# Optimization experiments

Measured on AMD Instinct MI355X. Metric: run time of the kernel, lower is better.

Reference implementation:

```python
import jax, jax.numpy as jnp
import numpy as np

N, E, G = 100000, 1600000, 64   # nodes, edges, graphs
IN, H, OUT = 32, 128, 3


def setup_inputs() -> dict:
    key = jax.random.key(0)
    ks = jax.random.split(key, 24)
    def w(k, i, o):
        return (jax.random.normal(k, (i, o), jnp.float32) / np.sqrt(i)).astype(jnp.float32)
    inp = {
        "x": jax.random.normal(ks[0], (N, IN), jnp.float32),
        "edge_index": jax.random.randint(ks[1], (2, E), 0, N, dtype=jnp.int32).astype(jnp.int64),
        "batch": jnp.sort(jax.random.randint(ks[2], (N,), 0, G, dtype=jnp.int32)).astype(jnp.int64),
        # SAGEConv layer 0 (in->hidden): lin_l (neighbors, with bias), lin_r (root, no bias)
        "Wl0": w(ks[3], IN, H), "bl0": jnp.zeros((H,), jnp.float32), "Wr0": w(ks[4], IN, H),
        # SAGEConv layers 1,2 (hidden->hidden)
        "Wl1": w(ks[5], H, H), "bl1": jnp.zeros((H,), jnp.float32), "Wr1": w(ks[6], H, H),
        "Wl2": w(ks[7], H, H), "bl2": jnp.zeros((H,), jnp.float32), "Wr2": w(ks[8], H, H),
        # output head
        "Wfc": w(ks[9], H, OUT), "bfc": jnp.zeros((OUT,), jnp.float32),
        # aux MLP on (dim1, dim3)
        "Wa1": w(ks[10], 2, H), "ba1": jnp.zeros((H,), jnp.float32),
        "Wa2": w(ks[11], H, H), "ba2": jnp.zeros((H,), jnp.float32),
        "Wao": w(ks[12], H, 1), "bao": jnp.zeros((1,), jnp.float32),
    }
    return inp


def _sage_conv(x, src, dst, Wl, bl, Wr):
    # PyG SAGEConv (mean aggr): out = lin_l(mean_{j in N(i)} x_j) + lin_r(x_i)
    msg = x[src]                                   # [E, d] gather
    agg = jax.ops.segment_sum(msg, dst, num_segments=N)
    cnt = jax.ops.segment_sum(jnp.ones((src.shape[0],), x.dtype), dst, num_segments=N)
    mean = agg / jnp.maximum(cnt, 1.0)[:, None]
    return mean @ Wl + bl + x @ Wr


def reference(x, edge_index, batch,
              Wl0, bl0, Wr0, Wl1, bl1, Wr1, Wl2, bl2, Wr2,
              Wfc, bfc, Wa1, ba1, Wa2, ba2, Wao, bao):
    src, dst = edge_index[0], edge_index[1]
    h = jax.nn.relu(_sage_conv(x, src, dst, Wl0, bl0, Wr0))   # dropout is identity in eval
    h = jax.nn.relu(_sage_conv(h, src, dst, Wl1, bl1, Wr1))
    h = jax.nn.relu(_sage_conv(h, src, dst, Wl2, bl2, Wr2))
    main = h @ Wfc + bfc                                      # [N, 3]
    dim1, dim3 = main[:, 0], main[:, 2]
    aux_in = jnp.stack([dim1, dim3], axis=-1)                 # [N, 2]
    a = jax.nn.relu(aux_in @ Wa1 + ba1)
    a = jax.nn.relu(a @ Wa2 + ba2)
    aux_out = (a @ Wao + bao)[:, 0]                           # [N]
    final = jnp.stack([dim1, aux_out, dim3], axis=-1)         # [N, 3]
    # global mean pool over graph ids
    s = jax.ops.segment_sum(final, batch, num_segments=G)
    c = jax.ops.segment_sum(jnp.ones((final.shape[0],), final.dtype), batch, num_segments=G)
    return s / jnp.maximum(c, 1.0)[:, None]                   # [G, 3]
```

## Files before the change

kernel.cpp:

```cpp
#include <hip/hip_runtime.h>

#define NR 128
#define PART_CH 4096
typedef unsigned short ushortT;
typedef __attribute__((ext_vector_type(8))) short short8;
typedef __attribute__((ext_vector_type(4))) float float4v;
typedef __attribute__((ext_vector_type(2))) float float2v;

__device__ __forceinline__ unsigned short f32_to_bf16_rne(float f) {
    unsigned u = __float_as_uint(f);
    unsigned r = (u + 0x7fffu + ((u >> 16) & 1u)) >> 16;
    return (unsigned short)r;
}

__device__ __forceinline__ unsigned char f32_to_fp8(float f) {
    return (unsigned char)(__builtin_amdgcn_cvt_pk_fp8_f32(f, f, 0, false) & 0xff);
}

__device__ __forceinline__ void accum8(float* acc, uint4 v) {
    unsigned u[4] = {v.x, v.y, v.z, v.w};
#pragma unroll
    for (int q = 0; q < 4; q++) {
        acc[2 * q]     += __uint_as_float(u[q] << 16);
        acc[2 * q + 1] += __uint_as_float(u[q] & 0xffff0000u);
    }
}

__device__ __forceinline__ void accum32_fp8(float* ag, uint4 A, uint4 B) {
    unsigned w[8] = {A.x, A.y, A.z, A.w, B.x, B.y, B.z, B.w};
#pragma unroll
    for (int m = 0; m < 8; m++) {
        float2v lo = __builtin_amdgcn_cvt_pk_f32_fp8(w[m], false);
        float2v hi = __builtin_amdgcn_cvt_pk_f32_fp8(w[m], true);
        ag[4 * m + 0] += lo.x;
        ag[4 * m + 1] += lo.y;
        ag[4 * m + 2] += hi.x;
        ag[4 * m + 3] += hi.y;
    }
}


__launch_bounds__(256)
__global__ void bucket_count(const int* __restrict__ dst, int* __restrict__ bcnt, int E, int NB) {
    __shared__ int h[1024];
    int t = threadIdx.x;
    for (int j = t; j < NB; j += 256) h[j] = 0;
    __syncthreads();
    int e0 = blockIdx.x * PART_CH;
    int e1 = min(e0 + PART_CH, E);
    for (int base = e0; base < e1; base += 2048) {
        int idx = base + t;
        int d[8];
        int cnt = 0;
#pragma unroll
        for (int u = 0; u < 8; u++) {
            int e = idx + u * 256;
            if (e < e1) d[cnt++] = dst[e];
        }
        for (int u = 0; u < cnt; u++) atomicAdd(&h[d[u] >> 7], 1);
    }
    __syncthreads();
    for (int j = t; j < NB; j += 256) {
        int v = h[j];
        if (v) atomicAdd(&bcnt[j], v);
    }
}

__launch_bounds__(256)
__global__ void bucket_scan(const int* __restrict__ bcnt, int* __restrict__ bstart,
                            int* __restrict__ gcur, int NB, int E) {
    __shared__ int sh[256];
    int t = threadIdx.x;
    int v[4];
    int tot = 0;
#pragma unroll
    for (int j = 0; j < 4; j++) {
        int idx = t * 4 + j;
        v[j] = (idx < NB) ? bcnt[idx] : 0;
        tot += v[j];
    }
    sh[t] = tot;
    __syncthreads();
    for (int off = 1; off < 256; off <<= 1) {
        int add = (t >= off) ? sh[t - off] : 0;
        __syncthreads();
        sh[t] += add;
        __syncthreads();
    }
    int run = sh[t] - tot;
#pragma unroll
    for (int j = 0; j < 4; j++) {
        int idx = t * 4 + j;
        if (idx < NB) { bstart[idx] = run; gcur[idx] = run; }
        run += v[j];
    }
    if (t == 0) bstart[NB] = E;
}

__launch_bounds__(256)
__global__ void partition_edges(const int* __restrict__ src, const int* __restrict__ dst,
                                int* __restrict__ gcur, unsigned* __restrict__ packed,
                                int E, int NB) {
    __shared__ int hist[1024];
    __shared__ int base[1024];
    int t = threadIdx.x;
    int e0 = blockIdx.x * PART_CH;
    int e1 = min(e0 + PART_CH, E);
    for (int j = t; j < NB; j += 256) hist[j] = 0;
    __syncthreads();
    for (int bb = e0; bb < e1; bb += 2048) {
        int idx = bb + t;
        int d[8];
        int cnt = 0;
#pragma unroll
        for (int u = 0; u < 8; u++) {
            int e = idx + u * 256;
            if (e < e1) d[cnt++] = dst[e];
        }
        for (int u = 0; u < cnt; u++) atomicAdd(&hist[d[u] >> 7], 1);
    }
    __syncthreads();
    for (int j = t; j < NB; j += 256) {
        int h = hist[j];
        base[j] = h ? atomicAdd(&gcur[j], h) : 0;
    }
    __syncthreads();
    for (int j = t; j < NB; j += 256) hist[j] = base[j];
    __syncthreads();
    for (int bb = e0; bb < e1; bb += 2048) {
        int idx = bb + t;
        int d[8], s[8];
        int cnt = 0;
#pragma unroll
        for (int u = 0; u < 8; u++) {
            int e = idx + u * 256;
            if (e < e1) { d[cnt] = dst[e]; s[cnt] = src[e]; cnt++; }
        }
        for (int u = 0; u < cnt; u++) {
            int dd = d[u];
            int pos = atomicAdd(&hist[dd >> 7], 1);
            packed[pos] = (unsigned)s[u] | ((unsigned)(dd & (NR - 1)) << 17);
        }
    }
}

__launch_bounds__(256)
__global__ void bucket_sort(const unsigned* __restrict__ packed, const int* __restrict__ bstart,
                            int* __restrict__ row_start, int* __restrict__ srcs, int N) {
    __shared__ int cnt[1024];
    __shared__ int cur[1024];
    __shared__ int psum[256];
    int b = blockIdx.x, t = threadIdx.x;
    int nb0 = b * NR;
    int nnode = min(NR, N - nb0);
    int lo = bstart[b], hi = bstart[b + 1];
#pragma unroll
    for (int j = 0; j < 4; j++) cnt[t + j * 256] = 0;
    __syncthreads();
    for (int bb = lo; bb < hi; bb += 2048) {
        int idx = bb + t;
        unsigned pk[8];
        int c = 0;
#pragma unroll
        for (int u = 0; u < 8; u++) {
            int e = idx + u * 256;
            if (e < hi) pk[c++] = packed[e];
        }
        for (int u = 0; u < c; u++) {
            unsigned s = pk[u] & 0x1FFFFu;
            int key = (int)((pk[u] >> 17) << 3) | (int)(s >> 14);
            atomicAdd(&cnt[key], 1);
        }
    }
    __syncthreads();
    int base4 = t * 4;
    int v0 = cnt[base4], v1 = cnt[base4 + 1], v2 = cnt[base4 + 2], v3 = cnt[base4 + 3];
    int s4 = v0 + v1 + v2 + v3;
    psum[t] = s4;
    __syncthreads();
    for (int off = 1; off < 256; off <<= 1) {
        int add = (t >= off) ? psum[t - off] : 0;
        __syncthreads();
        psum[t] += add;
        __syncthreads();
    }
    int run = psum[t] - s4;
    cnt[base4]     = run;
    cnt[base4 + 1] = run + v0;
    cnt[base4 + 2] = run + v0 + v1;
    cnt[base4 + 3] = run + v0 + v1 + v2;
    cur[base4]     = lo + run;
    cur[base4 + 1] = lo + run + v0;
    cur[base4 + 2] = lo + run + v0 + v1;
    cur[base4 + 3] = lo + run + v0 + v1 + v2;
    __syncthreads();
    if (t < nnode) row_start[nb0 + t] = lo + cnt[t << 3];
    if (t == 0 && nb0 + nnode == N) row_start[N] = hi;
    __syncthreads();
    for (int bb = lo; bb < hi; bb += 2048) {
        int idx = bb + t;
        unsigned pk[8];
        int c = 0;
#pragma unroll
        for (int u = 0; u < 8; u++) {
            int e = idx + u * 256;
            if (e < hi) pk[c++] = packed[e];
        }
        for (int u = 0; u < c; u++) {
            unsigned s = pk[u] & 0x1FFFFu;
            int key = (int)((pk[u] >> 17) << 3) | (int)(s >> 14);
            int pos = atomicAdd(&cur[key], 1);
            srcs[pos] = (int)s;
        }
    }
}


__global__ void prep_fused(const float* __restrict__ x, ushortT* __restrict__ xbf, int n4,
                           const float* __restrict__ Wl0, const float* __restrict__ Wr0,
                           const float* __restrict__ Wl1, const float* __restrict__ Wr1,
                           const float* __restrict__ Wl2, const float* __restrict__ Wr2,
                           const float* __restrict__ Wa2,
                           ushortT* __restrict__ Wt0, ushortT* __restrict__ Wt1,
                           ushortT* __restrict__ Wt2, ushortT* __restrict__ Wa2t) {
    int tid0 = blockIdx.x * 256 + threadIdx.x;
    if (tid0 < n4) {
        float4 v = ((const float4*)x)[tid0];
        ushort4 o;
        o.x = f32_to_bf16_rne(v.x);
        o.y = f32_to_bf16_rne(v.y);
        o.z = f32_to_bf16_rne(v.z);
        o.w = f32_to_bf16_rne(v.w);
        ((ushort4*)xbf)[tid0] = o;
        return;
    }
    int tid = tid0 - n4;
    if (tid < 8192) {
        int col = tid >> 6, k = tid & 63;
        float v = (k < 32) ? Wl0[k * 128 + col] : Wr0[(k - 32) * 128 + col];
        Wt0[col * 64 + ((k + 8 * col) & 63)] = f32_to_bf16_rne(v);
    } else if (tid < 8192 + 32768) {
        int j = tid - 8192;
        int col = j >> 8, k = j & 255;
        float v = (k < 128) ? Wl1[k * 128 + col] : Wr1[(k - 128) * 128 + col];
        Wt1[(k >> 6) * 8192 + col * 64 + (((k & 63) + 8 * col) & 63)] = f32_to_bf16_rne(v);
    } else if (tid < 8192 + 65536) {
        int j = tid - 8192 - 32768;
        int col = j >> 8, k = j & 255;
        float v = (k < 128) ? Wl2[k * 128 + col] : Wr2[(k - 128) * 128 + col];
        Wt2[(k >> 6) * 8192 + col * 64 + (((k & 63) + 8 * col) & 63)] = f32_to_bf16_rne(v);
    } else if (tid < 8192 + 65536 + 16384) {
        int j = tid - 8192 - 65536;
        int col = j >> 7, k = j & 127;
        Wa2t[(k >> 6) * 8192 + col * 64 + (((k & 63) + 8 * col) & 63)] = f32_to_bf16_rne(Wa2[k * 128 + col]);
    }
}


__device__ __forceinline__ void gather_fp8(const uint4* __restrict__ hp,
                                           const int* __restrict__ srcs,
                                           int lo, int deg, int q, float* ag) {
    if (deg <= 0) return;
    int last = lo + deg - 1;
    int nb = (deg + 3) >> 2;
    int sA[4], sB[4];
    uint4 A[8], B[8];
#pragma unroll
    for (int u = 0; u < 4; u++) sA[u] = srcs[min(lo + u, last)];
#pragma unroll
    for (int u = 0; u < 4; u++) {
        size_t bs = (size_t)sA[u] * 8 + q * 2;
        A[2 * u] = hp[bs];
        A[2 * u + 1] = hp[bs + 1];
    }
#pragma unroll
    for (int u = 0; u < 4; u++) sB[u] = srcs[min(lo + 4 + u, last)];
    for (int b = 0; b < nb; b += 2) {
#pragma unroll
        for (int u = 0; u < 4; u++) {
            size_t bs = (size_t)sB[u] * 8 + q * 2;
            B[2 * u] = hp[bs];
            B[2 * u + 1] = hp[bs + 1];
        }
#pragma unroll
        for (int u = 0; u < 4; u++) sA[u] = srcs[min(lo + (b + 2) * 4 + u, last)];
        {
            int rem = deg - b * 4;
#pragma unroll
            for (int u = 0; u < 4; u++)
                if (u < rem) accum32_fp8(ag, A[2 * u], A[2 * u + 1]);
        }
#pragma unroll
        for (int u = 0; u < 4; u++) {
            size_t bs = (size_t)sA[u] * 8 + q * 2;
            A[2 * u] = hp[bs];
            A[2 * u + 1] = hp[bs + 1];
        }
#pragma unroll
        for (int u = 0; u < 4; u++) sB[u] = srcs[min(lo + (b + 3) * 4 + u, last)];
        {
            int rem = deg - (b + 1) * 4;
#pragma unroll
            for (int u = 0; u < 4; u++)
                if (u < rem) accum32_fp8(ag, B[2 * u], B[2 * u + 1]);
        }
    }
}

__device__ __forceinline__ void gather_bf16(const uint4* __restrict__ xp,
                                            const int* __restrict__ srcs,
                                            int lo, int deg, int q, float* ag) {
    if (deg <= 0) return;
    int last = lo + deg - 1;
    int nb = (deg + 7) >> 3;
    int sA[8], sB[8];
    uint4 A[8], B[8];
#pragma unroll
    for (int u = 0; u < 8; u++) sA[u] = srcs[min(lo + u, last)];
#pragma unroll
    for (int u = 0; u < 8; u++) A[u] = xp[(size_t)sA[u] * 4 + q];
#pragma unroll
    for (int u = 0; u < 8; u++) sB[u] = srcs[min(lo + 8 + u, last)];
    for (int b = 0; b < nb; b += 2) {
#pragma unroll
        for (int u = 0; u < 8; u++) B[u] = xp[(size_t)sB[u] * 4 + q];
#pragma unroll
        for (int u = 0; u < 8; u++) sA[u] = srcs[min(lo + (b + 2) * 8 + u, last)];
        {
            int rem = deg - b * 8;
#pragma unroll
            for (int u = 0; u < 8; u++)
                if (u < rem) accum8(ag, A[u]);
        }
#pragma unroll
        for (int u = 0; u < 8; u++) A[u] = xp[(size_t)sA[u] * 4 + q];
#pragma unroll
        for (int u = 0; u < 8; u++) sB[u] = srcs[min(lo + (b + 3) * 8 + u, last)];
        {
            int rem = deg - (b + 1) * 8;
#pragma unroll
            for (int u = 0; u < 8; u++)
                if (u < rem) accum8(ag, B[u]);
        }
    }
}


__device__ __forceinline__ void stage_copy(ushortT* sW, const ushortT* Wq, int t) {
    const uint4* Wg = (const uint4*)Wq;
    uint4* Ws = (uint4*)sW;
#pragma unroll
    for (int j = 0; j < 4; j++) Ws[t + j * 256] = Wg[t + j * 256];
}

template <int KH, bool IN_FP8>
__device__ __forceinline__ void gemm_agg_body(
        const void* __restrict__ gat, const ushortT* __restrict__ Ah,
        const int* __restrict__ srcs, const int* __restrict__ rs,
        const ushortT* __restrict__ Wt, const float* __restrict__ bias,
        ushortT* __restrict__ outbf, unsigned char* __restrict__ outf8, int n) {
    constexpr int NKS = KH / 32;
    __shared__ __attribute__((aligned(16))) ushortT sW[128 * 64];
    int t = threadIdx.x;
    stage_copy(sW, Wt, t);
    int wv = t >> 6, lane = t & 63;
    int q = lane >> 4, cid = lane & 15;
    int row = blockIdx.x * 64 + wv * 16 + cid;
    int rc = min(row, n - 1);

    float ag[NKS * 8];
#pragma unroll
    for (int j = 0; j < NKS * 8; j++) ag[j] = 0.f;
    int lo = rs[rc], deg = rs[rc + 1] - lo;
    if constexpr (IN_FP8) gather_fp8((const uint4*)gat, srcs, lo, deg, q, ag);
    else                  gather_bf16((const uint4*)gat, srcs, lo, deg, q, ag);
    float inv = 1.0f / (float)max(deg, 1);
    short8 am[NKS];
#pragma unroll
    for (int ks = 0; ks < NKS; ks++)
#pragma unroll
        for (int j = 0; j < 8; j++) am[ks][j] = (short)f32_to_bf16_rne(ag[ks * 8 + j] * inv);
    short8 ah[NKS];
#pragma unroll
    for (int ks = 0; ks < NKS; ks++)
        ah[ks] = *(const short8*)(Ah + (size_t)rc * KH + ks * 32 + q * 8);
    __syncthreads();

    float4v acc[8];
#pragma unroll
    for (int j = 0; j < 8; j++) acc[j] = (float4v){0.f, 0.f, 0.f, 0.f};
    int pbase = q * 8 + 8 * cid;
    if constexpr (KH == 32) {
        {
            int p = pbase & 63;
#pragma unroll
            for (int j = 0; j < 8; ++j) {
                short8 b = *(const short8*)(sW + (j * 16 + cid) * 64 + p);
                acc[j] = __builtin_amdgcn_mfma_f32_16x16x32_bf16(am[0], b, acc[j], 0, 0, 0);
            }
        }
        {
            int p = (32 + pbase) & 63;
#pragma unroll
            for (int j = 0; j < 8; ++j) {
                short8 b = *(const short8*)(sW + (j * 16 + cid) * 64 + p);
                acc[j] = __builtin_amdgcn_mfma_f32_16x16x32_bf16(ah[0], b, acc[j], 0, 0, 0);
            }
        }
    } else {
#pragma unroll
        for (int st = 0; st < 4; st++) {
            if (st > 0) {
                __syncthreads();
                stage_copy(sW, Wt + st * 8192, t);
                __syncthreads();
            }
#pragma unroll
            for (int ksl = 0; ksl < 2; ksl++) {
                short8 a = (st < 2) ? am[st * 2 + ksl] : ah[(st - 2) * 2 + ksl];
                int p = (ksl * 32 + pbase) & 63;
#pragma unroll
                for (int j = 0; j < 8; ++j) {
                    short8 b = *(const short8*)(sW + (j * 16 + cid) * 64 + p);
                    acc[j] = __builtin_amdgcn_mfma_f32_16x16x32_bf16(a, b, acc[j], 0, 0, 0);
                }
            }
        }
    }
    float bo[8];
#pragma unroll
    for (int j = 0; j < 8; ++j) bo[j] = bias[j * 16 + cid];
    int orow = blockIdx.x * 64 + wv * 16 + q * 4;
#pragma unroll
    for (int rr = 0; rr < 4; ++rr) {
        int r = orow + rr;
        if (r < n) {
#pragma unroll
            for (int j = 0; j < 8; ++j) {
                int col = j * 16 + cid;
                float v = fmaxf(acc[j][rr] + bo[j], 0.f);
                outbf[(size_t)r * 128 + col] = f32_to_bf16_rne(v);
                int pc = ((col >> 3) & 3) * 32 + ((col >> 5) << 3) + (col & 7);
                outf8[(size_t)r * 128 + pc] = f32_to_fp8(v);
            }
        }
    }
}

__launch_bounds__(256, 2)
__global__ void gemm_agg32(const void* __restrict__ gat, const ushortT* __restrict__ Ah,
                           const int* __restrict__ srcs, const int* __restrict__ rs,
                           const ushortT* __restrict__ Wt, const float* __restrict__ bias,
                           ushortT* __restrict__ outbf, unsigned char* __restrict__ outf8, int n) {
    gemm_agg_body<32, false>(gat, Ah, srcs, rs, Wt, bias, outbf, outf8, n);
}

__launch_bounds__(256, 2)
__global__ void gemm_agg128(const void* __restrict__ gat, const ushortT* __restrict__ Ah,
                            const int* __restrict__ srcs, const int* __restrict__ rs,
                            const ushortT* __restrict__ Wt, const float* __restrict__ bias,
                            ushortT* __restrict__ outbf, unsigned char* __restrict__ outf8, int n) {
    gemm_agg_body<128, true>(gat, Ah, srcs, rs, Wt, bias, outbf, outf8, n);
}


__launch_bounds__(256, 2)
__global__ void gemm_agg_fin(const void* __restrict__ gat, const ushortT* __restrict__ Ah,
                             const int* __restrict__ srcs, const int* __restrict__ rs,
                             const ushortT* __restrict__ Wt, const float* __restrict__ bias,
                             const float* __restrict__ Wfc, const float* __restrict__ bfc,
                             const ushortT* __restrict__ Wa2t, const float* __restrict__ Wa1,
                             const float* __restrict__ ba1, const float* __restrict__ ba2,
                             const float* __restrict__ Wao, const float* __restrict__ bao,
                             float* __restrict__ fin, int n) {
    __shared__ __attribute__((aligned(16))) ushortT sW[128 * 64];
    __shared__ float sD1[64], sD3[64];
    __shared__ float sWa1a[128], sWa1b[128], sBa1[128];
    int t = threadIdx.x;
    stage_copy(sW, Wt, t);
    if (t < 128) { sWa1a[t] = Wa1[t]; sWa1b[t] = Wa1[128 + t]; sBa1[t] = ba1[t]; }
    int wv = t >> 6, lane = t & 63;
    int q = lane >> 4, cid = lane & 15;
    int row = blockIdx.x * 64 + wv * 16 + cid;
    int rc = min(row, n - 1);

    float ag[32];
#pragma unroll
    for (int j = 0; j < 32; j++) ag[j] = 0.f;
    int lo = rs[rc], deg = rs[rc + 1] - lo;
    gather_fp8((const uint4*)gat, srcs, lo, deg, q, ag);
    float inv = 1.0f / (float)max(deg, 1);
    short8 am[4];
#pragma unroll
    for (int ks = 0; ks < 4; ks++)
#pragma unroll
        for (int j = 0; j < 8; j++) am[ks][j] = (short)f32_to_bf16_rne(ag[ks * 8 + j] * inv);
    short8 ah[4];
#pragma unroll
    for (int ks = 0; ks < 4; ks++)
        ah[ks] = *(const short8*)(Ah + (size_t)rc * 128 + ks * 32 + q * 8);
    __syncthreads();

    float4v acc[8];
#pragma unroll
    for (int j = 0; j < 8; j++) acc[j] = (float4v){0.f, 0.f, 0.f, 0.f};
    int pbase = q * 8 + 8 * cid;
#pragma unroll
    for (int st = 0; st < 4; st++) {
        if (st > 0) {
            __syncthreads();
            stage_copy(sW, Wt + st * 8192, t);
            __syncthreads();
        }
#pragma unroll
        for (int ksl = 0; ksl < 2; ksl++) {
            short8 a = (st < 2) ? am[st * 2 + ksl] : ah[(st - 2) * 2 + ksl];
            int p = (ksl * 32 + pbase) & 63;
#pragma unroll
            for (int j = 0; j < 8; ++j) {
                short8 b = *(const short8*)(sW + (j * 16 + cid) * 64 + p);
                acc[j] = __builtin_amdgcn_mfma_f32_16x16x32_bf16(a, b, acc[j], 0, 0, 0);
            }
        }
    }

    float bo[8], w1[8], w3[8];
#pragma unroll
    for (int j = 0; j < 8; ++j) {
        int col = j * 16 + cid;
        bo[j] = bias[col];
        w1[j] = Wfc[col * 3 + 0];
        w3[j] = Wfc[col * 3 + 2];
    }
    float bfc0 = bfc[0], bfc2 = bfc[2];
#pragma unroll
    for (int rr = 0; rr < 4; ++rr) {
        float p1 = 0.f, p3 = 0.f;
#pragma unroll
        for (int j = 0; j < 8; ++j) {
            float v = fmaxf(acc[j][rr] + bo[j], 0.f);
            p1 += v * w1[j];
            p3 += v * w3[j];
        }
        p1 += __shfl_xor(p1, 1, 64); p3 += __shfl_xor(p3, 1, 64);
        p1 += __shfl_xor(p1, 2, 64); p3 += __shfl_xor(p3, 2, 64);
        p1 += __shfl_xor(p1, 4, 64); p3 += __shfl_xor(p3, 4, 64);
        p1 += __shfl_xor(p1, 8, 64); p3 += __shfl_xor(p3, 8, 64);
        if (cid == 0) {
            int rowl = wv * 16 + q * 4 + rr;
            float d1 = p1 + bfc0, d3 = p3 + bfc2;
            sD1[rowl] = d1;
            sD3[rowl] = d3;
            int r = blockIdx.x * 64 + rowl;
            if (r < n) {
                fin[(size_t)r * 3 + 0] = d1;
                fin[(size_t)r * 3 + 2] = d3;
            }
        }
    }
    __syncthreads();

    int rl = wv * 16 + cid;
    float d1a = sD1[rl], d3a = sD3[rl];
    float4v hacc[8];
#pragma unroll
    for (int j = 0; j < 8; j++) hacc[j] = (float4v){0.f, 0.f, 0.f, 0.f};
#pragma unroll
    for (int hs = 0; hs < 2; hs++) {
        if (hs > 0) __syncthreads();
        stage_copy(sW, Wa2t + hs * 8192, t);
        __syncthreads();
#pragma unroll
        for (int ksl = 0; ksl < 2; ++ksl) {
            int k0 = hs * 64 + ksl * 32 + q * 8;
            short8 a0;
#pragma unroll
            for (int j = 0; j < 8; ++j) {
                int k = k0 + j;
                float v0 = fmaxf(fmaf(d1a, sWa1a[k], fmaf(d3a, sWa1b[k], sBa1[k])), 0.f);
                a0[j] = (short)f32_to_bf16_rne(v0);
            }
            int p = (ksl * 32 + pbase) & 63;
#pragma unroll
            for (int j = 0; j < 8; ++j) {
                short8 b = *(const short8*)(sW + (j * 16 + cid) * 64 + p);
                hacc[j] = __builtin_amdgcn_mfma_f32_16x16x32_bf16(a0, b, hacc[j], 0, 0, 0);
            }
        }
    }
    float b2[8], wo[8];
#pragma unroll
    for (int j = 0; j < 8; ++j) {
        int col = j * 16 + cid;
        b2[j] = ba2[col];
        wo[j] = Wao[col];
    }
    float bao0 = bao[0];
#pragma unroll
    for (int rr = 0; rr < 4; ++rr) {
        float s = 0.f;
#pragma unroll
        for (int j = 0; j < 8; ++j) s += fmaxf(hacc[j][rr] + b2[j], 0.f) * wo[j];
        s += __shfl_xor(s, 1, 64);
        s += __shfl_xor(s, 2, 64);
        s += __shfl_xor(s, 4, 64);
        s += __shfl_xor(s, 8, 64);
        int r = blockIdx.x * 64 + wv * 16 + q * 4 + rr;
        if (cid == 0 && r < n) fin[(size_t)r * 3 + 1] = s + bao0;
    }
}


__global__ void pool_kernel(const float* __restrict__ fin, const int* __restrict__ batch,
                            float* __restrict__ out, int n) {
    int g = blockIdx.x, t = threadIdx.x;
    int lo = 0, hi = n;
    while (lo < hi) { int mid = (lo + hi) >> 1; if (batch[mid] < g) lo = mid + 1; else hi = mid; }
    int start = lo;
    lo = 0; hi = n;
    while (lo < hi) { int mid = (lo + hi) >> 1; if (batch[mid] < g + 1) lo = mid + 1; else hi = mid; }
    int end = lo;
    float s0 = 0.f, s1 = 0.f, s2 = 0.f;
    for (int i = start + t; i < end; i += 256) {
        s0 += fin[(size_t)i * 3 + 0];
        s1 += fin[(size_t)i * 3 + 1];
        s2 += fin[(size_t)i * 3 + 2];
    }
    __shared__ float r0[256], r1[256], r2[256];
    r0[t] = s0; r1[t] = s1; r2[t] = s2;
    __syncthreads();
    for (int off = 128; off > 0; off >>= 1) {
        if (t < off) { r0[t] += r0[t + off]; r1[t] += r1[t + off]; r2[t] += r2[t + off]; }
        __syncthreads();
    }
    if (t == 0) {
        float c = (float)max(end - start, 1);
        out[g * 3 + 0] = r0[0] / c;
        out[g * 3 + 1] = r1[0] / c;
        out[g * 3 + 2] = r2[0] / c;
    }
}


extern "C" void kernel_launch(void* const* d_in, const int* in_sizes, int n_in,
                              void* d_out, int out_size, void* d_ws, size_t ws_size,
                              hipStream_t stream) {
    const float* x    = (const float*)d_in[0];
    const int*   ei   = (const int*)d_in[1];
    const int*   batch= (const int*)d_in[2];
    const float* Wl0  = (const float*)d_in[3];
    const float* bl0  = (const float*)d_in[4];
    const float* Wr0  = (const float*)d_in[5];
    const float* Wl1  = (const float*)d_in[6];
    const float* bl1  = (const float*)d_in[7];
    const float* Wr1  = (const float*)d_in[8];
    const float* Wl2  = (const float*)d_in[9];
    const float* bl2  = (const float*)d_in[10];
    const float* Wr2  = (const float*)d_in[11];
    const float* Wfc  = (const float*)d_in[12];
    const float* bfc  = (const float*)d_in[13];
    const float* Wa1  = (const float*)d_in[14];
    const float* ba1  = (const float*)d_in[15];
    const float* Wa2  = (const float*)d_in[16];
    const float* ba2  = (const float*)d_in[17];
    const float* Wao  = (const float*)d_in[18];
    const float* bao  = (const float*)d_in[19];

    const int N = in_sizes[0] / 32;
    const int E = in_sizes[1] / 2;
    const int G = out_size / 3;
    const int* src = ei;
    const int* dst = ei + E;
    float* out = (float*)d_out;
    const int NB = (N + NR - 1) / NR;

    char* p = (char*)d_ws;
    auto carve = [&](size_t bytes) {
        void* r = (void*)p;
        p += (bytes + 255) & ~(size_t)255;
        return r;
    };
    int*           bcnt     = (int*)carve((size_t)NB * 4);
    int*           bstart   = (int*)carve((size_t)(NB + 1) * 4);
    int*           gcur     = (int*)carve((size_t)NB * 4);
    int*           row_start= (int*)carve((size_t)(N + 1) * 4);
    unsigned*      packed   = (unsigned*)carve((size_t)E * 4);
    int*           srcs     = (int*)carve((size_t)E * 4);
    ushortT*       xbf      = (ushortT*)carve((size_t)N * 32 * 2);
    ushortT*       hbf0     = (ushortT*)carve((size_t)N * 128 * 2);
    ushortT*       hbf1     = (ushortT*)carve((size_t)N * 128 * 2);
    unsigned char* hf8_0    = (unsigned char*)carve((size_t)N * 128);
    unsigned char* hf8_1    = (unsigned char*)carve((size_t)N * 128);
    float*         fin      = (float*)carve((size_t)N * 3 * 4);
    ushortT*       Wt0      = (ushortT*)carve((size_t)128 * 64 * 2);
    ushortT*       Wt1      = (ushortT*)carve((size_t)128 * 256 * 2);
    ushortT*       Wt2      = (ushortT*)carve((size_t)128 * 256 * 2);
    ushortT*       Wa2t     = (ushortT*)carve((size_t)128 * 128 * 2);

    const int gemm_grid = (N + 63) / 64;
    const int part_grid = (E + PART_CH - 1) / PART_CH;
    const int n4 = N * 32 / 4;

    prep_fused<<<(n4 + 90112 + 255) / 256, 256, 0, stream>>>(
        x, xbf, n4, Wl0, Wr0, Wl1, Wr1, Wl2, Wr2, Wa2, Wt0, Wt1, Wt2, Wa2t);

    hipMemsetAsync(bcnt, 0, (size_t)NB * 4, stream);
    bucket_count<<<part_grid, 256, 0, stream>>>(dst, bcnt, E, NB);
    bucket_scan<<<1, 256, 0, stream>>>(bcnt, bstart, gcur, NB, E);
    partition_edges<<<part_grid, 256, 0, stream>>>(src, dst, gcur, packed, E, NB);
    bucket_sort<<<NB, 256, 0, stream>>>(packed, bstart, row_start, srcs, N);

    gemm_agg32<<<gemm_grid, 256, 0, stream>>>(
        (const void*)xbf, xbf, srcs, row_start, Wt0, bl0, hbf0, hf8_0, N);
    gemm_agg128<<<gemm_grid, 256, 0, stream>>>(
        (const void*)hf8_0, hbf0, srcs, row_start, Wt1, bl1, hbf1, hf8_1, N);
    gemm_agg_fin<<<gemm_grid, 256, 0, stream>>>(
        (const void*)hf8_1, hbf1, srcs, row_start, Wt2, bl2, Wfc, bfc,
        Wa2t, Wa1, ba1, ba2, Wao, bao, fin, N);

    pool_kernel<<<G, 256, 0, stream>>>(fin, batch, out, N);
}
```

Before: 350.6 us.

## Split neighbor gather across two wave halves per row with LDS reduction

Blocks grow from 256 to 512 threads. Each node's edge list is split between two groups of four waves, and the second half writes its partial sums to shared memory for the first half to add. Only the first half then runs the MFMA GEMM and the epilogue. The aim is more memory-level parallelism in the latency-bound gather, at the cost of extra LDS per block (about 33–66 KB), another barrier, and half the waves idling during the GEMM, which may lower occupancy.

```diff
diff --git a/kernel.cpp b/kernel.cpp
--- a/kernel.cpp
+++ b/kernel.cpp
@@ -346,11 +346,11 @@
 }
 
 
-__device__ __forceinline__ void stage_copy(ushortT* sW, const ushortT* Wq, int t) {
+__device__ __forceinline__ void stage_copy2(ushortT* sW, const ushortT* Wq, int t) {
     const uint4* Wg = (const uint4*)Wq;
     uint4* Ws = (uint4*)sW;
-#pragma unroll
-    for (int j = 0; j < 4; j++) Ws[t + j * 256] = Wg[t + j * 256];
+    Ws[t] = Wg[t];
+    Ws[t + 512] = Wg[t + 512];
 }
 
 template <int KH, bool IN_FP8>
@@ -360,51 +360,69 @@
         const ushortT* __restrict__ Wt, const float* __restrict__ bias,
         ushortT* __restrict__ outbf, unsigned char* __restrict__ outf8, int n) {
     constexpr int NKS = KH / 32;
+    constexpr int PJ = NKS * 8 + 1;
     __shared__ __attribute__((aligned(16))) ushortT sW[128 * 64];
+    __shared__ float pL[256 * PJ];
     int t = threadIdx.x;
-    stage_copy(sW, Wt, t);
-    int wv = t >> 6, lane = t & 63;
+    stage_copy2(sW, Wt, t);
+    int wave = t >> 6, lane = t & 63;
+    int half = wave >> 2, wv = wave & 3;
     int q = lane >> 4, cid = lane & 15;
-    int row = blockIdx.x * 64 + wv * 16 + cid;
+    int row_local = wv * 16 + cid;
+    int row = blockIdx.x * 64 + row_local;
     int rc = min(row, n - 1);
 
     float ag[NKS * 8];
 #pragma unroll
     for (int j = 0; j < NKS * 8; j++) ag[j] = 0.f;
     int lo = rs[rc], deg = rs[rc + 1] - lo;
-    if constexpr (IN_FP8) gather_fp8((const uint4*)gat, srcs, lo, deg, q, ag);
-    else                  gather_bf16((const uint4*)gat, srcs, lo, deg, q, ag);
-    float inv = 1.0f / (float)max(deg, 1);
-    short8 am[NKS];
-#pragma unroll
-    for (int ks = 0; ks < NKS; ks++)
-#pragma unroll
-        for (int j = 0; j < 8; j++) am[ks][j] = (short)f32_to_bf16_rne(ag[ks * 8 + j] * inv);
-    short8 ah[NKS];
-#pragma unroll
-    for (int ks = 0; ks < NKS; ks++)
-        ah[ks] = *(const short8*)(Ah + (size_t)rc * KH + ks * 32 + q * 8);
-    __syncthreads();
+    int d0 = (deg + 1) >> 1;
+    int mylo = half ? lo + d0 : lo;
+    int mydeg = half ? deg - d0 : d0;
+    if constexpr (IN_FP8) gather_fp8((const uint4*)gat, srcs, mylo, mydeg, q, ag);
+    else                  gather_bf16((const uint4*)gat, srcs, mylo, mydeg, q, ag);
+    int r4q = row_local * 4 + q;
+    if (half) {
+#pragma unroll
+        for (int j = 0; j < NKS * 8; j++) pL[r4q * PJ + j] = ag[j];
+    }
+    __syncthreads();
+
+    short8 am[NKS], ah[NKS];
+    if (!half) {
+#pragma unroll
+        for (int j = 0; j < NKS * 8; j++) ag[j] += pL[r4q * PJ + j];
+        float inv = 1.0f / (float)max(deg, 1);
+#pragma unroll
+        for (int ks = 0; ks < NKS; ks++)
+#pragma unroll
+            for (int j = 0; j < 8; j++) am[ks][j] = (short)f32_to_bf16_rne(ag[ks * 8 + j] * inv);
+#pragma unroll
+        for (int ks = 0; ks < NKS; ks++)
+            ah[ks] = *(const short8*)(Ah + (size_t)rc * KH + ks * 32 + q * 8);
+    }
 
     float4v acc[8];
 #pragma unroll
     for (int j = 0; j < 8; j++) acc[j] = (float4v){0.f, 0.f, 0.f, 0.f};
     int pbase = q * 8 + 8 * cid;
     if constexpr (KH == 32) {
-        {
-            int p = pbase & 63;
-#pragma unroll
-            for (int j = 0; j < 8; ++j) {
-                short8 b = *(const short8*)(sW + (j * 16 + cid) * 64 + p);
-                acc[j] = __builtin_amdgcn_mfma_f32_16x16x32_bf16(am[0], b, acc[j], 0, 0, 0);
-            }
-        }
-        {
-            int p = (32 + pbase) & 63;
-#pragma unroll
-            for (int j = 0; j < 8; ++j) {
-                short8 b = *(const short8*)(sW + (j * 16 + cid) * 64 + p);
-                acc[j] = __builtin_amdgcn_mfma_f32_16x16x32_bf16(ah[0], b, acc[j], 0, 0, 0);
+        if (!half) {
+            {
+                int p = pbase & 63;
+#pragma unroll
+                for (int j = 0; j < 8; ++j) {
+                    short8 b = *(const short8*)(sW + (j * 16 + cid) * 64 + p);
+                    acc[j] = __builtin_amdgcn_mfma_f32_16x16x32_bf16(am[0], b, acc[j], 0, 0, 0);
+                }
+            }
+            {
+                int p = (32 + pbase) & 63;
+#pragma unroll
+                for (int j = 0; j < 8; ++j) {
+                    short8 b = *(const short8*)(sW + (j * 16 + cid) * 64 + p);
+                    acc[j] = __builtin_amdgcn_mfma_f32_16x16x32_bf16(ah[0], b, acc[j], 0, 0, 0);
+                }
             }
         }
     } else {
@@ -412,42 +430,46 @@
         for (int st = 0; st < 4; st++) {
             if (st > 0) {
                 __syncthreads();
-                stage_copy(sW, Wt + st * 8192, t);
+                stage_copy2(sW, Wt + st * 8192, t);
                 __syncthreads();
             }
-#pragma unroll
-            for (int ksl = 0; ksl < 2; ksl++) {
-                short8 a = (st < 2) ? am[st * 2 + ksl] : ah[(st - 2) * 2 + ksl];
-                int p = (ksl * 32 + pbase) & 63;
+            if (!half) {
+#pragma unroll
+                for (int ksl = 0; ksl < 2; ksl++) {
+                    short8 a = (st < 2) ? am[st * 2 + ksl] : ah[(st - 2) * 2 + ksl];
+                    int p = (ksl * 32 + pbase) & 63;
+#pragma unroll
+                    for (int j = 0; j < 8; ++j) {
+                        short8 b = *(const short8*)(sW + (j * 16 + cid) * 64 + p);
+                        acc[j] = __builtin_amdgcn_mfma_f32_16x16x32_bf16(a, b, acc[j], 0, 0, 0);
+                    }
+                }
+            }
+        }
+    }
+    if (!half) {
+        float bo[8];
+#pragma unroll
+        for (int j = 0; j < 8; ++j) bo[j] = bias[j * 16 + cid];
+        int orow = blockIdx.x * 64 + wv * 16 + q * 4;
+#pragma unroll
+        for (int rr = 0; rr < 4; ++rr) {
+            int r = orow + rr;
+            if (r < n) {
 #pragma unroll
                 for (int j = 0; j < 8; ++j) {
-                    short8 b = *(const short8*)(sW + (j * 16 + cid) * 64 + p);
-                    acc[j] = __builtin_amdgcn_mfma_f32_16x16x32_bf16(a, b, acc[j], 0, 0, 0);
+                    int col = j * 16 + cid;
+                    float v = fmaxf(acc[j][rr] + bo[j], 0.f);
+                    outbf[(size_t)r * 128 + col] = f32_to_bf16_rne(v);
+                    int pc = ((col >> 3) & 3) * 32 + ((col >> 5) << 3) + (col & 7);
+                    outf8[(size_t)r * 128 + pc] = f32_to_fp8(v);
                 }
             }
         }
     }
-    float bo[8];
-#pragma unroll
-    for (int j = 0; j < 8; ++j) bo[j] = bias[j * 16 + cid];
-    int orow = blockIdx.x * 64 + wv * 16 + q * 4;
-#pragma unroll
-    for (int rr = 0; rr < 4; ++rr) {
-        int r = orow + rr;
-        if (r < n) {
-#pragma unroll
-            for (int j = 0; j < 8; ++j) {
-                int col = j * 16 + cid;
-                float v = fmaxf(acc[j][rr] + bo[j], 0.f);
-                outbf[(size_t)r * 128 + col] = f32_to_bf16_rne(v);
-                int pc = ((col >> 3) & 3) * 32 + ((col >> 5) << 3) + (col & 7);
-                outf8[(size_t)r * 128 + pc] = f32_to_fp8(v);
-            }
-        }
-    }
-}
-
-__launch_bounds__(256, 2)
+}
+
+__launch_bounds__(512, 2)
 __global__ void gemm_agg32(const void* __restrict__ gat, const ushortT* __restrict__ Ah,
                            const int* __restrict__ srcs, const int* __restrict__ rs,
                            const ushortT* __restrict__ Wt, const float* __restrict__ bias,
@@ -455,7 +477,7 @@
     gemm_agg_body<32, false>(gat, Ah, srcs, rs, Wt, bias, outbf, outf8, n);
 }
 
-__launch_bounds__(256, 2)
+__launch_bounds__(512, 2)
 __global__ void gemm_agg128(const void* __restrict__ gat, const ushortT* __restrict__ Ah,
                             const int* __restrict__ srcs, const int* __restrict__ rs,
                             const ushortT* __restrict__ Wt, const float* __restrict__ bias,
@@ -464,7 +486,7 @@
 }
 
 
-__launch_bounds__(256, 2)
+__launch_bounds__(512, 2)
 __global__ void gemm_agg_fin(const void* __restrict__ gat, const ushortT* __restrict__ Ah,
                              const int* __restrict__ srcs, const int* __restrict__ rs,
                              const ushortT* __restrict__ Wt, const float* __restrict__ bias,
@@ -473,33 +495,49 @@
                              const float* __restrict__ ba1, const float* __restrict__ ba2,
                              const float* __restrict__ Wao, const float* __restrict__ bao,
                              float* __restrict__ fin, int n) {
+    constexpr int PJ = 33;
     __shared__ __attribute__((aligned(16))) ushortT sW[128 * 64];
+    __shared__ float pL[256 * PJ];
     __shared__ float sD1[64], sD3[64];
     __shared__ float sWa1a[128], sWa1b[128], sBa1[128];
     int t = threadIdx.x;
-    stage_copy(sW, Wt, t);
+    stage_copy2(sW, Wt, t);
     if (t < 128) { sWa1a[t] = Wa1[t]; sWa1b[t] = Wa1[128 + t]; sBa1[t] = ba1[t]; }
-    int wv = t >> 6, lane = t & 63;
+    int wave = t >> 6, lane = t & 63;
+    int half = wave >> 2, wv = wave & 3;
     int q = lane >> 4, cid = lane & 15;
-    int row = blockIdx.x * 64 + wv * 16 + cid;
+    int row_local = wv * 16 + cid;
+    int row = blockIdx.x * 64 + row_local;
     int rc = min(row, n - 1);
 
     float ag[32];
 #pragma unroll
     for (int j = 0; j < 32; j++) ag[j] = 0.f;
     int lo = rs[rc], deg = rs[rc + 1] - lo;
-    gather_fp8((const uint4*)gat, srcs, lo, deg, q, ag);
-    float inv = 1.0f / (float)max(deg, 1);
-    short8 am[4];
-#pragma unroll
-    for (int ks = 0; ks < 4; ks++)
-#pragma unroll
-        for (int j = 0; j < 8; j++) am[ks][j] = (short)f32_to_bf16_rne(ag[ks * 8 + j] * inv);
-    short8 ah[4];
-#pragma unroll
-    for (int ks = 0; ks < 4; ks++)
-        ah[ks] = *(const short8*)(Ah + (size_t)rc * 128 + ks * 32 + q * 8);
-    __syncthreads();
+    int d0 = (deg + 1) >> 1;
+    int mylo = half ? lo + d0 : lo;
+    int mydeg = half ? deg - d0 : d0;
+    gather_fp8((const uint4*)gat, srcs, mylo, mydeg, q, ag);
+    int r4q = row_local * 4 + q;
+    if (half) {
+#pragma unroll
+        for (int j = 0; j < 32; j++) pL[r4q * PJ + j] = ag[j];
+    }
+    __syncthreads();
+
+    short8 am[4], ah[4];
+    if (!half) {
+#pragma unroll
+        for (int j = 0; j < 32; j++) ag[j] += pL[r4q * PJ + j];
+        float inv = 1.0f / (float)max(deg, 1);
+#pragma unroll
+        for (int ks = 0; ks < 4; ks++)
+#pragma unroll
+            for (int j = 0; j < 8; j++) am[ks][j] = (short)f32_to_bf16_rne(ag[ks * 8 + j] * inv);
+#pragma unroll
+        for (int ks = 0; ks < 4; ks++)
+            ah[ks] = *(const short8*)(Ah + (size_t)rc * 128 + ks * 32 + q * 8);
+    }
 
     float4v acc[8];
 #pragma unroll
@@ -509,104 +547,112 @@
     for (int st = 0; st < 4; st++) {
         if (st > 0) {
             __syncthreads();
-            stage_copy(sW, Wt + st * 8192, t);
+            stage_copy2(sW, Wt + st * 8192, t);
             __syncthreads();
         }
-#pragma unroll
-        for (int ksl = 0; ksl < 2; ksl++) {
-            short8 a = (st < 2) ? am[st * 2 + ksl] : ah[(st - 2) * 2 + ksl];
-            int p = (ksl * 32 + pbase) & 63;
+        if (!half) {
+#pragma unroll
+            for (int ksl = 0; ksl < 2; ksl++) {
+                short8 a = (st < 2) ? am[st * 2 + ksl] : ah[(st - 2) * 2 + ksl];
+                int p = (ksl * 32 + pbase) & 63;
+#pragma unroll
+                for (int j = 0; j < 8; ++j) {
+                    short8 b = *(const short8*)(sW + (j * 16 + cid) * 64 + p);
+                    acc[j] = __builtin_amdgcn_mfma_f32_16x16x32_bf16(a, b, acc[j], 0, 0, 0);
+                }
+            }
+        }
+    }
+
+    if (!half) {
+        float bo[8], w1[8], w3[8];
+#pragma unroll
+        for (int j = 0; j < 8; ++j) {
+            int col = j * 16 + cid;
+            bo[j] = bias[col];
+            w1[j] = Wfc[col * 3 + 0];
+            w3[j] = Wfc[col * 3 + 2];
+        }
+        float bfc0 = bfc[0], bfc2 = bfc[2];
+#pragma unroll
+        for (int rr = 0; rr < 4; ++rr) {
+            float p1 = 0.f, p3 = 0.f;
 #pragma unroll
             for (int j = 0; j < 8; ++j) {
-                short8 b = *(const short8*)(sW + (j * 16 + cid) * 64 + p);
-                acc[j] = __builtin_amdgcn_mfma_f32_16x16x32_bf16(a, b, acc[j], 0, 0, 0);
-            }
-        }
-    }
-
-    float bo[8], w1[8], w3[8];
-#pragma unroll
-    for (int j = 0; j < 8; ++j) {
-        int col = j * 16 + cid;
-        bo[j] = bias[col];
-        w1[j] = Wfc[col * 3 + 0];
-        w3[j] = Wfc[col * 3 + 2];
-    }
-    float bfc0 = bfc[0], bfc2 = bfc[2];
-#pragma unroll
-    for (int rr = 0; rr < 4; ++rr) {
-        float p1 = 0.f, p3 = 0.f;
-#pragma unroll
-        for (int j = 0; j < 8; ++j) {
-            float v = fmaxf(acc[j][rr] + bo[j], 0.f);
-            p1 += v * w1[j];
-            p3 += v * w3[j];
-        }
-        p1 += __shfl_xor(p1, 1, 64); p3 += __shfl_xor(p3, 1, 64);
-        p1 += __shfl_xor(p1, 2, 64); p3 += __shfl_xor(p3, 2, 64);
-        p1 += __shfl_xor(p1, 4, 64); p3 += __shfl_xor(p3, 4, 64);
-        p1 += __shfl_xor(p1, 8, 64); p3 += __shfl_xor(p3, 8, 64);
-        if (cid == 0) {
-            int rowl = wv * 16 + q * 4 + rr;
-            float d1 = p1 + bfc0, d3 = p3 + bfc2;
-            sD1[rowl] = d1;
-            sD3[rowl] = d3;
-            int r = blockIdx.x * 64 + rowl;
-            if (r < n) {
-                fin[(size_t)r * 3 + 0] = d1;
-                fin[(size_t)r * 3 + 2] = d3;
-            }
-        }
-    }
-    __syncthreads();
-
-    int rl = wv * 16 + cid;
-    float d1a = sD1[rl], d3a = sD3[rl];
+                float v = fmaxf(acc[j][rr] + bo[j], 0.f);
+                p1 += v * w1[j];
+                p3 += v * w3[j];
+            }
+            p1 += __shfl_xor(p1, 1, 64); p3 += __shfl_xor(p3, 1, 64);
+            p1 += __shfl_xor(p1, 2, 64); p3 += __shfl_xor(p3, 2, 64);
+            p1 += __shfl_xor(p1, 4, 64); p3 += __shfl_xor(p3, 4, 64);
+            p1 += __shfl_xor(p1, 8, 64); p3 += __shfl_xor(p3, 8, 64);
+            if (cid == 0) {
+                int rowl = wv * 16 + q * 4 + rr;
+                float d1 = p1 + bfc0, d3 = p3 + bfc2;
+                sD1[rowl] = d1;
+                sD3[rowl] = d3;
+                int r = blockIdx.x * 64 + rowl;
+                if (r < n) {
+                    fin[(size_t)r * 3 + 0] = d1;
+                    fin[(size_t)r * 3 + 2] = d3;
+                }
+            }
+        }
+    }
+    __syncthreads();
+
+    float d1a = 0.f, d3a = 0.f;
+    if (!half) { d1a = sD1[row_local]; d3a = sD3[row_local]; }
     float4v hacc[8];
 #pragma unroll
     for (int j = 0; j < 8; j++) hacc[j] = (float4v){0.f, 0.f, 0.f, 0.f};
 #pragma unroll
     for (int hs = 0; hs < 2; hs++) {
         if (hs > 0) __syncthreads();
-        stage_copy(sW, Wa2t + hs * 8192, t);
+        stage_copy2(sW, Wa2t + hs * 8192, t);
         __syncthreads();
-#pragma unroll
-        for (int ksl = 0; ksl < 2; ++ksl) {
-            int k0 = hs * 64 + ksl * 32 + q * 8;
-            short8 a0;
-#pragma unroll
-            for (int j = 0; j < 8; ++j) {
-                int k = k0 + j;
-                float v0 = fmaxf(fmaf(d1a, sWa1a[k], fmaf(d3a, sWa1b[k], sBa1[k])), 0.f);
-                a0[j] = (short)f32_to_bf16_rne(v0);
-            }
-            int p = (ksl * 32 + pbase) & 63;
-#pragma unroll
-            for (int j = 0; j < 8; ++j) {
-                short8 b = *(const short8*)(sW + (j * 16 + cid) * 64 + p);
-                hacc[j] = __builtin_amdgcn_mfma_f32_16x16x32_bf16(a0, b, hacc[j], 0, 0, 0);
-            }
-        }
-    }
-    float b2[8], wo[8];
-#pragma unroll
-    for (int j = 0; j < 8; ++j) {
-        int col = j * 16 + cid;
-        b2[j] = ba2[col];
-        wo[j] = Wao[col];
-    }
-    float bao0 = bao[0];
-#pragma unroll
-    for (int rr = 0; rr < 4; ++rr) {
-        float s = 0.f;
-#pragma unroll
-        for (int j = 0; j < 8; ++j) s += fmaxf(hacc[j][rr] + b2[j], 0.f) * wo[j];
-        s += __shfl_xor(s, 1, 64);
-        s += __shfl_xor(s, 2, 64);
-        s += __shfl_xor(s, 4, 64);
-        s += __shfl_xor(s, 8, 64);
-        int r = blockIdx.x * 64 + wv * 16 + q * 4 + rr;
-        if (cid == 0 && r < n) fin[(size_t)r * 3 + 1] = s + bao0;
+        if (!half) {
+#pragma unroll
+            for (int ksl = 0; ksl < 2; ++ksl) {
+                int k0 = hs * 64 + ksl * 32 + q * 8;
+                short8 a0;
+#pragma unroll
+                for (int j = 0; j < 8; ++j) {
+                    int k = k0 + j;
+                    float v0 = fmaxf(fmaf(d1a, sWa1a[k], fmaf(d3a, sWa1b[k], sBa1[k])), 0.f);
+                    a0[j] = (short)f32_to_bf16_rne(v0);
+                }
+                int p = (ksl * 32 + pbase) & 63;
+#pragma unroll
+                for (int j = 0; j < 8; ++j) {
+                    short8 b = *(const short8*)(sW + (j * 16 + cid) * 64 + p);
+                    hacc[j] = __builtin_amdgcn_mfma_f32_16x16x32_bf16(a0, b, hacc[j], 0, 0, 0);
+                }
+            }
+        }
+    }
+    if (!half) {
+        float b2[8], wo[8];
+#pragma unroll
+        for (int j = 0; j < 8; ++j) {
+            int col = j * 16 + cid;
+            b2[j] = ba2[col];
+            wo[j] = Wao[col];
+        }
+        float bao0 = bao[0];
+#pragma unroll
+        for (int rr = 0; rr < 4; ++rr) {
+            float s = 0.f;
+#pragma unroll
+            for (int j = 0; j < 8; ++j) s += fmaxf(hacc[j][rr] + b2[j], 0.f) * wo[j];
+            s += __shfl_xor(s, 1, 64);
+            s += __shfl_xor(s, 2, 64);
+            s += __shfl_xor(s, 4, 64);
+            s += __shfl_xor(s, 8, 64);
+            int r = blockIdx.x * 64 + wv * 16 + q * 4 + rr;
+            if (cid == 0 && r < n) fin[(size_t)r * 3 + 1] = s + bao0;
+        }
     }
 }
 
@@ -710,11 +756,11 @@
     partition_edges<<<part_grid, 256, 0, stream>>>(src, dst, gcur, packed, E, NB);
     bucket_sort<<<NB, 256, 0, stream>>>(packed, bstart, row_start, srcs, N);
 
-    gemm_agg32<<<gemm_grid, 256, 0, stream>>>(
+    gemm_agg32<<<gemm_grid, 512, 0, stream>>>(
         (const void*)xbf, xbf, srcs, row_start, Wt0, bl0, hbf0, hf8_0, N);
-    gemm_agg128<<<gemm_grid, 256, 0, stream>>>(
+    gemm_agg128<<<gemm_grid, 512, 0, stream>>>(
         (const void*)hf8_0, hbf0, srcs, row_start, Wt1, bl1, hbf1, hf8_1, N);
-    gemm_agg_fin<<<gemm_grid, 256, 0, stream>>>(
+    gemm_agg_fin<<<gemm_grid, 512, 0, stream>>>(
         (const void*)hf8_1, hbf1, srcs, row_start, Wt2, bl2, Wfc, bfc,
         Wa2t, Wa1, ba1, ba2, Wao, bao, fin, N);
 
```

Measured after the change: 437.3 us. 1.25x slower.
